# Kernel optimization log

Hardware: AMD Instinct MI355X
Metric: run time of the kernel (lower is better)

Reference implementation:

```python
import jax, jax.numpy as jnp
import numpy as np

EPS = 1e-5

def conv3x3(x, w, b):
    # x: [B,C,H,W], w: [O,I,3,3]
    y = jax.lax.conv_general_dilated(x, w, window_strides=(1, 1),
                                     padding=((1, 1), (1, 1)),
                                     dimension_numbers=('NCHW', 'OIHW', 'NCHW'))
    return y + b[None, :, None, None]

def batchnorm(x, gamma, beta):
    # training-mode BN: batch stats over (N,H,W), biased variance
    mean = jnp.mean(x, axis=(0, 2, 3), keepdims=True)
    var = jnp.mean((x - mean) ** 2, axis=(0, 2, 3), keepdims=True)
    xn = (x - mean) * jax.lax.rsqrt(var + EPS)
    return xn * gamma[None, :, None, None] + beta[None, :, None, None]

def setup_inputs() -> dict:
    key = jax.random.key(0)
    ks = jax.random.split(key, 5)
    B, C, H, W = 4, 256, 64, 64
    fan = C * 9
    return {
        'x': jax.random.normal(ks[0], (B, C, H, W), jnp.float32),
        'wv': jax.random.normal(ks[1], (C, C, 3, 3), jnp.float32) / np.sqrt(fan),
        'bv': jax.random.normal(ks[2], (C,), jnp.float32) * 0.01,
        'gv': jnp.ones((C,), jnp.float32),
        'betav': jnp.zeros((C,), jnp.float32),
        'ww': jax.random.normal(ks[3], (C, C, 3, 3), jnp.float32) / np.sqrt(fan),
        'bw': jax.random.normal(ks[4], (C,), jnp.float32) * 0.01,
        'gw': jnp.ones((C,), jnp.float32),
        'betaw': jnp.zeros((C,), jnp.float32),
    }

def reference(x, wv, bv, gv, betav, ww, bw, gw, betaw):
    B, C, H, W = x.shape
    N = H * W
    # value branch: conv3x3 + BN -> [B, N, C]
    value = batchnorm(conv3x3(x, wv, bv), gv, betav).reshape(B, C, N)
    key_ = x.reshape(B, C, N)              # [B, C, N]
    query = key_.transpose(0, 2, 1)        # [B, N, C]
    sim = jnp.einsum('bnc,bcm->bnm', query, key_) * (C ** -0.5)  # [B, N, N]
    sim = jax.nn.softmax(sim, axis=-1)
    context = jnp.einsum('bnm,bcm->bcn', sim, value)             # [B, C, N]
    context = context.reshape(B, C, H, W)
    out = jax.nn.relu(batchnorm(conv3x3(context, ww, bw), gw, betaw))
    return out
```

## Files before the change

kernel.cpp:

```cpp
#include <hip/hip_runtime.h>
#include <cstdint>
#include <cstddef>

typedef __attribute__((ext_vector_type(8))) __bf16 bf16x8;
typedef __attribute__((ext_vector_type(4))) __bf16 bf16x4;
typedef __attribute__((ext_vector_type(4))) float  f32x4;

#define NPIX 4096
#define CHN  256

__device__ __forceinline__ void async_copy16(void* lds, const void* g) {
  __builtin_amdgcn_global_load_lds(
      (const __attribute__((address_space(1))) unsigned int*)g,
      (__attribute__((address_space(3))) unsigned int*)lds, 16, 0, 0);
}

__global__ __launch_bounds__(256) void k_transpose_cast(
    const float* __restrict__ X, __bf16* __restrict__ xT)
{
  __shared__ float tile[64][65];
  const int bid = blockIdx.x;
  const int b  = bid >> 8;
  const int pt = (bid >> 2) & 63;
  const int ct = bid & 3;
  const int tid = threadIdx.x;
  const int tc = tid & 63, tr = tid >> 6;
  const float* Xb = X + ((size_t)b*CHN + ct*64)*NPIX + pt*64;
#pragma unroll
  for (int i=0;i<16;++i) {
    int row = tr + i*4;
    tile[row][tc] = Xb[(size_t)row*NPIX + tc];
  }
  __syncthreads();
  __bf16* Tb = xT + ((size_t)b*NPIX + pt*64)*CHN + ct*64;
#pragma unroll
  for (int i=0;i<16;++i) {
    int prow = tr + i*4;
    Tb[(size_t)prow*CHN + tc] = (__bf16)tile[tc][prow];
  }
}

__global__ __launch_bounds__(256) void k_wcast(
    const float* __restrict__ wv, const float* __restrict__ ww,
    __bf16* __restrict__ wvt, __bf16* __restrict__ wwt)
{
  int idx = blockIdx.x*256 + threadIdx.x;
  int t = idx >> 16;
  int o = (idx >> 8) & 255;
  int i = idx & 255;
  size_t src = ((size_t)o*256 + i)*9 + t;
  wvt[idx] = (__bf16)wv[src];
  wwt[idx] = (__bf16)ww[src];
}

__global__ __launch_bounds__(512, 1) void k_conv_tap(
    const __bf16* __restrict__ W9,
    const __bf16* __restrict__ Bt,
    const __bf16* __restrict__ zb,
    __bf16* __restrict__ Y)
{
  __shared__ __bf16 Alds[2][128*64];
  __shared__ __bf16 Blds[2][128*64];
  const int bid0 = blockIdx.x;
  const int bid = (bid0 & 7)*32 + (bid0 >> 3);
  const int b  = bid >> 6;
  const int mt = (bid >> 5) & 1;
  const int nt = bid & 31;
  const int m0 = mt << 7;
  const int p0 = nt << 7;
  const int tid = threadIdx.x;
  const int w = tid >> 6, l = tid & 63;
  const int l15 = l & 15, lhi = l >> 4;
  const int wr = (w >> 1) << 5;
  const int wc = (w & 1) << 6;

  const __bf16* Btb = Bt + ((size_t)b << 20);
  const f32x4 vzero = {0.f,0.f,0.f,0.f};
  f32x4 acc[2][4];
#pragma unroll
  for (int i=0;i<2;++i)
#pragma unroll
    for (int j=0;j<4;++j) acc[i][j] = vzero;

  auto stage = [&](int buf, int it) {
    const int t = it >> 2, kc = it & 3;
    const int dy = t/3 - 1, dx = t%3 - 1;
    const int dq = dy*64 + dx;
    const int k0 = kc << 6;
#pragma unroll
    for (int i=0;i<2;++i) {
      int inst = w*2 + i;
      int s = inst*64 + l;
      int row = s >> 3, ch = s & 7;
      const __bf16* g = W9 + (size_t)t*65536 + (size_t)(m0+row)*256 + k0
                        + ((ch ^ (row & 7)) << 3);
      async_copy16((char*)(&Alds[buf][0]) + inst*1024, g);
    }
#pragma unroll
    for (int i=0;i<2;++i) {
      int inst = w*2 + i;
      int s = inst*64 + l;
      int pp = s >> 3, ch = s & 7;
      int p = p0 + pp;
      int xx = (p & 63) + dx;
      int yy = (p >> 6) + dy;
      bool ok = ((unsigned)xx < 64u) & ((unsigned)yy < 64u);
      const __bf16* g = ok ? (Btb + (size_t)(p + dq)*256 + k0 + ((ch ^ (pp & 7)) << 3))
                           : zb;
      async_copy16((char*)(&Blds[buf][0]) + inst*1024, g);
    }
  };

  stage(0, 0);
#pragma unroll 1
  for (int it=0; it<36; ++it) {
    const int cur = it & 1;
    if (it < 35) {
      stage(cur^1, it+1);
      asm volatile("s_waitcnt vmcnt(4)" ::: "memory");
    } else {
      asm volatile("s_waitcnt vmcnt(0)" ::: "memory");
    }
    __builtin_amdgcn_s_barrier();
    __builtin_amdgcn_sched_barrier(0);

    const char* Ac = (const char*)(&Alds[cur][0]);
    const char* Bc = (const char*)(&Blds[cur][0]);
#pragma unroll
    for (int kk=0; kk<2; ++kk) {
      const int swz = (((kk<<2)+lhi) ^ (l15 & 7)) << 4;
      bf16x8 af[2], bfr[4];
#pragma unroll
      for (int i=0;i<2;++i)
        af[i] = *(const bf16x8*)(Ac + (size_t)(wr + 16*i + l15)*128 + swz);
#pragma unroll
      for (int j=0;j<4;++j)
        bfr[j] = *(const bf16x8*)(Bc + (size_t)(wc + 16*j + l15)*128 + swz);
#pragma unroll
      for (int i=0;i<2;++i)
#pragma unroll
        for (int j=0;j<4;++j)
          acc[i][j] = __builtin_amdgcn_mfma_f32_16x16x32_bf16(af[i], bfr[j], acc[i][j], 0,0,0);
    }
    __builtin_amdgcn_s_barrier();
  }

  __bf16* Yb = Y + ((size_t)b << 20);
#pragma unroll
  for (int i=0;i<2;++i)
#pragma unroll
    for (int j=0;j<4;++j)
#pragma unroll
      for (int r=0;r<4;++r) {
        int row = m0 + wr + 16*i + lhi*4 + r;
        int col = p0 + wc + 16*j + l15;
        Yb[(size_t)row*NPIX + col] = (__bf16)acc[i][j][r];
      }
}

__global__ __launch_bounds__(256) void k_bn_stats(
    const __bf16* __restrict__ Y, const float* __restrict__ gamma,
    const float* __restrict__ beta, float* __restrict__ scale,
    float* __restrict__ shift)
{
  const int c = blockIdx.x;
  const int tid = threadIdx.x;
  float s = 0.f, s2 = 0.f;
#pragma unroll 1
  for (int b=0;b<4;++b) {
    const __bf16* p = Y + ((size_t)b*CHN + c)*NPIX;
#pragma unroll
    for (int i=0;i<2;++i) {
      bf16x8 v = *(const bf16x8*)(p + (tid + i*256)*8);
#pragma unroll
      for (int j=0;j<8;++j) { float f = (float)v[j]; s += f; s2 += f*f; }
    }
  }
#pragma unroll
  for (int d=1; d<64; d<<=1) { s += __shfl_xor(s, d, 64); s2 += __shfl_xor(s2, d, 64); }
  __shared__ float rs[4], rs2[4];
  if ((tid & 63) == 0) { rs[tid>>6] = s; rs2[tid>>6] = s2; }
  __syncthreads();
  if (tid == 0) {
    float S  = rs[0]+rs[1]+rs[2]+rs[3];
    float S2 = rs2[0]+rs2[1]+rs2[2]+rs2[3];
    const float inv_n = 1.f/16384.f;
    float mean = S*inv_n;
    float var  = S2*inv_n - mean*mean;
    float rstd = rsqrtf(var + 1e-5f);
    float sc = gamma[c]*rstd;
    scale[c] = sc;
    shift[c] = beta[c] - mean*sc;
  }
}

__global__ __launch_bounds__(256) void k_bn_relu(
    const __bf16* __restrict__ Y, const float* __restrict__ scale,
    const float* __restrict__ shift, float* __restrict__ out)
{
  size_t idx = ((size_t)blockIdx.x*256 + threadIdx.x)*8;
  int c = (int)((idx >> 12) & 255);
  bf16x8 v = *(const bf16x8*)(Y + idx);
  float sc = scale[c], sh = shift[c];
  float4 r0, r1;
  r0.x = fmaxf((float)v[0]*sc + sh, 0.f);
  r0.y = fmaxf((float)v[1]*sc + sh, 0.f);
  r0.z = fmaxf((float)v[2]*sc + sh, 0.f);
  r0.w = fmaxf((float)v[3]*sc + sh, 0.f);
  r1.x = fmaxf((float)v[4]*sc + sh, 0.f);
  r1.y = fmaxf((float)v[5]*sc + sh, 0.f);
  r1.z = fmaxf((float)v[6]*sc + sh, 0.f);
  r1.w = fmaxf((float)v[7]*sc + sh, 0.f);
  *(float4*)(out + idx)     = r0;
  *(float4*)(out + idx + 4) = r1;
}

__global__ __launch_bounds__(512, 2) void k_attn(
    const __bf16* __restrict__ xT,
    const __bf16* __restrict__ val,
    const float* __restrict__ scale,
    const float* __restrict__ shift,
    __bf16* __restrict__ O)
{
  __shared__ __align__(16) char smem[141312];

  const int bid0 = blockIdx.x;
  const int bid = (bid0 & 7)*32 + (bid0 >> 3);
  const int b  = bid >> 6;
  const int q0 = (bid & 63) << 6;
  const int tid = threadIdx.x;
  const int w = tid >> 6, l = tid & 63;
  const int l15 = l & 15, lhi = l >> 4;
  const int qh  = w & 1;
  const int kvq = w >> 1;
  const int p   = kvq >> 1;
  const int cfh = kvq & 1;

  const __bf16* xTb = xT  + ((size_t)b << 20);
  const __bf16* vb  = val + ((size_t)b << 20);

  bf16x8 aq[2][8];
#pragma unroll
  for (int rg=0; rg<2; ++rg) {
    const __bf16* qp = xTb + (size_t)(q0 + qh*32 + rg*16 + l15)*256 + lhi*8;
#pragma unroll
    for (int kc=0; kc<8; ++kc) {
      bf16x8 v = *(const bf16x8*)(qp + kc*32);
#pragma unroll
      for (int j=0;j<8;++j) v[j] = (__bf16)((float)v[j] * 0.0625f);
      aq[rg][kc] = v;
    }
  }

  auto stage = [&](int buf, int m0) {
    char* kb = smem + buf*32768;
    char* vv = smem + 65536 + buf*32768;
#pragma unroll
    for (int i=0;i<4;++i) {
      int inst = w*4 + i;
      int s = inst*64 + l;
      int row = s >> 5, cs = s & 31;
      const __bf16* g = xTb + (size_t)(m0 + row)*256 + ((cs ^ (row & 7)) << 3);
      async_copy16(kb + inst*1024, g);
    }
#pragma unroll
    for (int i=0;i<4;++i) {
      int inst = w*4 + i;
      int s = inst*64 + l;
      int row = s >> 3, cs = s & 7;
      const __bf16* g = vb + (size_t)row*NPIX + m0 + ((cs ^ (row & 7)) << 3);
      async_copy16(vv + inst*1024, g);
    }
  };

  const f32x4 vzero = {0.f,0.f,0.f,0.f};
  float lsum[2][4];
#pragma unroll
  for (int rg=0;rg<2;++rg)
#pragma unroll
    for (int r=0;r<4;++r) lsum[rg][r] = 0.f;
  f32x4 o[2][8];
#pragma unroll
  for (int rg=0;rg<2;++rg)
#pragma unroll
    for (int cf=0; cf<8; ++cf) o[rg][cf] = vzero;

  stage(0, 0);

#pragma unroll 1
  for (int mt=0; mt<64; ++mt) {
    const int cur = mt & 1;
    asm volatile("s_waitcnt vmcnt(0)" ::: "memory");
    __builtin_amdgcn_s_barrier();
    __builtin_amdgcn_sched_barrier(0);
    if (mt < 63) stage(cur^1, (mt+1) << 6);

    const char* Kc = smem + cur*32768;
    const char* Vc = smem + 65536 + cur*32768;
    __bf16* pReg = (__bf16*)(smem + 131072 + (qh*2 + p)*2560);

    f32x4 s4[2];
    s4[0] = vzero; s4[1] = vzero;
    {
      const int krow = kvq*16 + l15;
      const char* kbase = Kc + krow*512;
#pragma unroll
      for (int kc=0; kc<8; ++kc) {
        bf16x8 bk = *(const bf16x8*)(kbase + ((((kc<<2)+lhi) ^ (krow&7)) << 4));
        s4[0] = __builtin_amdgcn_mfma_f32_16x16x32_bf16(aq[0][kc], bk, s4[0], 0,0,0);
        s4[1] = __builtin_amdgcn_mfma_f32_16x16x32_bf16(aq[1][kc], bk, s4[1], 0,0,0);
      }
    }

#pragma unroll
    for (int rg=0;rg<2;++rg)
#pragma unroll
      for (int r=0;r<4;++r) {
        float pv = __expf(s4[rg][r]);
        __bf16 pbf = (__bf16)pv;
        pReg[(rg*16 + lhi*4 + r)*40 + cfh*16 + l15] = pbf;
        lsum[rg][r] += (float)pbf;
      }

    asm volatile("s_waitcnt lgkmcnt(0)" ::: "memory");
    __builtin_amdgcn_s_barrier();
    __builtin_amdgcn_sched_barrier(0);

    bf16x8 pa0 = *(const bf16x8*)(pReg + (size_t)l15*40 + lhi*8);
    bf16x8 pa1 = *(const bf16x8*)(pReg + (size_t)(16 + l15)*40 + lhi*8);

#pragma unroll
    for (int cf=0; cf<8; ++cf) {
      const int c = cfh*128 + (cf<<4) + l15;
      const char* vbase = Vc + c*128;
      bf16x8 bv = *(const bf16x8*)(vbase + ((((p<<2)+lhi) ^ (c&7)) << 4));
      o[0][cf] = __builtin_amdgcn_mfma_f32_16x16x32_bf16(pa0, bv, o[0][cf], 0,0,0);
      o[1][cf] = __builtin_amdgcn_mfma_f32_16x16x32_bf16(pa1, bv, o[1][cf], 0,0,0);
    }
  }

#pragma unroll
  for (int rg=0;rg<2;++rg)
#pragma unroll
    for (int r=0;r<4;++r)
#pragma unroll
      for (int d=1; d<16; d<<=1) lsum[rg][r] += __shfl_xor(lsum[rg][r], d, 64);

  __builtin_amdgcn_s_barrier();
  float* oscr = (float*)smem;
  float* lscr = (float*)(smem + 65536);
  if (l15 == 0) {
#pragma unroll
    for (int rg=0;rg<2;++rg)
#pragma unroll
      for (int r=0;r<4;++r)
        lscr[w*32 + rg*16 + lhi*4 + r] = lsum[rg][r];
  }
  if (p == 1) {
    float* od = oscr + (size_t)(qh*2 + cfh)*4096;
#pragma unroll
    for (int rg=0;rg<2;++rg)
#pragma unroll
      for (int cf=0;cf<8;++cf)
#pragma unroll
        for (int r=0;r<4;++r)
          od[(rg*16 + lhi*4 + r)*128 + (cf<<4) + l15] = o[rg][cf][r];
  }
  asm volatile("s_waitcnt lgkmcnt(0)" ::: "memory");
  __builtin_amdgcn_s_barrier();
  if (p == 0) {
    const float* od = oscr + (size_t)(qh*2 + cfh)*4096;
    __bf16* Ob = O + ((size_t)b << 20);
#pragma unroll
    for (int rg=0;rg<2;++rg) {
      float inv[4];
#pragma unroll
      for (int r=0;r<4;++r) {
        float tot = 0.f;
#pragma unroll
        for (int k=0;k<4;++k)
          tot += lscr[(qh + 2*k)*32 + rg*16 + lhi*4 + r];
        inv[r] = 1.f / tot;
      }
#pragma unroll
      for (int cf=0;cf<8;++cf) {
        const int c = cfh*128 + (cf<<4) + l15;
        const float sc = scale[c], sh = shift[c];
#pragma unroll
        for (int r=0;r<4;++r) {
          float vtot = o[rg][cf][r] + od[(rg*16 + lhi*4 + r)*128 + (cf<<4) + l15];
          int row = q0 + qh*32 + rg*16 + lhi*4 + r;
          Ob[(size_t)row*256 + c] = (__bf16)(vtot * inv[r] * sc + sh);
        }
      }
    }
  }
}

extern "C" void kernel_launch(void* const* d_in, const int* in_sizes, int n_in,
                              void* d_out, int out_size, void* d_ws, size_t ws_size,
                              hipStream_t stream)
{
  const float* x     = (const float*)d_in[0];
  const float* wv    = (const float*)d_in[1];
  const float* gv    = (const float*)d_in[3];
  const float* betav = (const float*)d_in[4];
  const float* ww    = (const float*)d_in[5];
  const float* gw    = (const float*)d_in[7];
  const float* betaw = (const float*)d_in[8];
  float* out = (float*)d_out;

  char* ws = (char*)d_ws;
  __bf16* xT     = (__bf16*)(ws);
  __bf16* Obuf   = (__bf16*)(ws + 8388608);
  __bf16* ybuf   = (__bf16*)(ws + 16777216);
  __bf16* wvt    = (__bf16*)(ws + 25165824);
  __bf16* wwt    = (__bf16*)(ws + 26345472);
  float* scale_v = (float*)(ws + 27525120);
  float* shift_v = (float*)(ws + 27526144);
  float* scale_w = (float*)(ws + 27527168);
  float* shift_w = (float*)(ws + 27528192);
  __bf16* zbuf   = (__bf16*)(ws + 27529216);
  if (ws_size < 27530240) return;

  hipMemsetAsync(zbuf, 0, 1024, stream);

  k_transpose_cast<<<1024, 256, 0, stream>>>(x, xT);
  k_wcast<<<2304, 256, 0, stream>>>(wv, ww, wvt, wwt);

  k_conv_tap<<<256, 512, 0, stream>>>(wvt, xT, zbuf, ybuf);
  k_bn_stats<<<256, 256, 0, stream>>>(ybuf, gv, betav, scale_v, shift_v);

  k_attn<<<256, 512, 0, stream>>>(xT, ybuf, scale_v, shift_v, Obuf);

  k_conv_tap<<<256, 512, 0, stream>>>(wwt, Obuf, zbuf, ybuf);
  k_bn_stats<<<256, 256, 0, stream>>>(ybuf, gw, betaw, scale_w, shift_w);
  k_bn_relu<<<2048, 256, 0, stream>>>(ybuf, scale_w, shift_w, out);
}
```

Baseline: 197.3 us.

## Fuse BN partial statistics into conv epilogue and finalize with tiny kernel

The conv kernel now accumulates per-channel sum and sum-of-squares of its bf16-rounded outputs, reduces them across lanes with shuffles, and writes per-tile partials to workspace. A single-block finalize kernel sums the 256 partials per channel to produce scale and shift. This replaces the separate BN stats kernel that re-read the whole 8MB conv output. It adds shuffle reductions to the conv epilogue and a serial 256-iteration loop in a one-block kernel.

```diff
diff --git a/kernel.cpp b/kernel.cpp
--- a/kernel.cpp
+++ b/kernel.cpp
@@ -57,7 +57,9 @@
     const __bf16* __restrict__ W9,
     const __bf16* __restrict__ Bt,
     const __bf16* __restrict__ zb,
-    __bf16* __restrict__ Y)
+    __bf16* __restrict__ Y,
+    float* __restrict__ PS,
+    float* __restrict__ PS2)
 {
   __shared__ __bf16 Alds[2][128*64];
   __shared__ __bf16 Blds[2][128*64];
@@ -146,6 +148,11 @@
   }
 
   __bf16* Yb = Y + ((size_t)b << 20);
+  float ps[2][4], ps2[2][4];
+#pragma unroll
+  for (int i=0;i<2;++i)
+#pragma unroll
+    for (int r=0;r<4;++r) { ps[i][r] = 0.f; ps2[i][r] = 0.f; }
 #pragma unroll
   for (int i=0;i<2;++i)
 #pragma unroll
@@ -154,44 +161,53 @@
       for (int r=0;r<4;++r) {
         int row = m0 + wr + 16*i + lhi*4 + r;
         int col = p0 + wc + 16*j + l15;
-        Yb[(size_t)row*NPIX + col] = (__bf16)acc[i][j][r];
-      }
-}
-
-__global__ __launch_bounds__(256) void k_bn_stats(
-    const __bf16* __restrict__ Y, const float* __restrict__ gamma,
-    const float* __restrict__ beta, float* __restrict__ scale,
-    float* __restrict__ shift)
-{
-  const int c = blockIdx.x;
-  const int tid = threadIdx.x;
-  float s = 0.f, s2 = 0.f;
-#pragma unroll 1
-  for (int b=0;b<4;++b) {
-    const __bf16* p = Y + ((size_t)b*CHN + c)*NPIX;
-#pragma unroll
-    for (int i=0;i<2;++i) {
-      bf16x8 v = *(const bf16x8*)(p + (tid + i*256)*8);
-#pragma unroll
-      for (int j=0;j<8;++j) { float f = (float)v[j]; s += f; s2 += f*f; }
-    }
-  }
-#pragma unroll
-  for (int d=1; d<64; d<<=1) { s += __shfl_xor(s, d, 64); s2 += __shfl_xor(s2, d, 64); }
-  __shared__ float rs[4], rs2[4];
-  if ((tid & 63) == 0) { rs[tid>>6] = s; rs2[tid>>6] = s2; }
-  __syncthreads();
-  if (tid == 0) {
-    float S  = rs[0]+rs[1]+rs[2]+rs[3];
-    float S2 = rs2[0]+rs2[1]+rs2[2]+rs2[3];
-    const float inv_n = 1.f/16384.f;
-    float mean = S*inv_n;
-    float var  = S2*inv_n - mean*mean;
-    float rstd = rsqrtf(var + 1e-5f);
-    float sc = gamma[c]*rstd;
-    scale[c] = sc;
-    shift[c] = beta[c] - mean*sc;
-  }
+        __bf16 vb16 = (__bf16)acc[i][j][r];
+        float v = (float)vb16;
+        ps[i][r]  += v;
+        ps2[i][r] += v*v;
+        Yb[(size_t)row*NPIX + col] = vb16;
+      }
+#pragma unroll
+  for (int i=0;i<2;++i)
+#pragma unroll
+    for (int r=0;r<4;++r)
+#pragma unroll
+      for (int d=1; d<16; d<<=1) {
+        ps[i][r]  += __shfl_xor(ps[i][r],  d, 64);
+        ps2[i][r] += __shfl_xor(ps2[i][r], d, 64);
+      }
+  if (l15 == 0) {
+    const int contrib = b*64 + nt*2 + (wc >> 6);
+#pragma unroll
+    for (int i=0;i<2;++i)
+#pragma unroll
+      for (int r=0;r<4;++r) {
+        int c = m0 + wr + 16*i + lhi*4 + r;
+        PS [contrib*256 + c] = ps[i][r];
+        PS2[contrib*256 + c] = ps2[i][r];
+      }
+  }
+}
+
+__global__ __launch_bounds__(256) void k_bn_finalize(
+    const float* __restrict__ PS, const float* __restrict__ PS2,
+    const float* __restrict__ gamma, const float* __restrict__ beta,
+    float* __restrict__ scale, float* __restrict__ shift)
+{
+  const int c = threadIdx.x;
+  float S = 0.f, S2 = 0.f;
+#pragma unroll 4
+  for (int k=0;k<256;++k) {
+    S  += PS [k*256 + c];
+    S2 += PS2[k*256 + c];
+  }
+  const float inv_n = 1.f/16384.f;
+  float mean = S*inv_n;
+  float var  = S2*inv_n - mean*mean;
+  float rstd = rsqrtf(var + 1e-5f);
+  float sc = gamma[c]*rstd;
+  scale[c] = sc;
+  shift[c] = beta[c] - mean*sc;
 }
 
 __global__ __launch_bounds__(256) void k_bn_relu(
@@ -421,19 +437,21 @@
   float* scale_w = (float*)(ws + 27527168);
   float* shift_w = (float*)(ws + 27528192);
   __bf16* zbuf   = (__bf16*)(ws + 27529216);
-  if (ws_size < 27530240) return;
+  float* part_s  = (float*)(ws + 27530240);
+  float* part_s2 = (float*)(ws + 27792384);
+  if (ws_size < 28054528) return;
 
   hipMemsetAsync(zbuf, 0, 1024, stream);
 
   k_transpose_cast<<<1024, 256, 0, stream>>>(x, xT);
   k_wcast<<<2304, 256, 0, stream>>>(wv, ww, wvt, wwt);
 
-  k_conv_tap<<<256, 512, 0, stream>>>(wvt, xT, zbuf, ybuf);
-  k_bn_stats<<<256, 256, 0, stream>>>(ybuf, gv, betav, scale_v, shift_v);
+  k_conv_tap<<<256, 512, 0, stream>>>(wvt, xT, zbuf, ybuf, part_s, part_s2);
+  k_bn_finalize<<<1, 256, 0, stream>>>(part_s, part_s2, gv, betav, scale_v, shift_v);
 
   k_attn<<<256, 512, 0, stream>>>(xT, ybuf, scale_v, shift_v, Obuf);
 
-  k_conv_tap<<<256, 512, 0, stream>>>(wwt, Obuf, zbuf, ybuf);
-  k_bn_stats<<<256, 256, 0, stream>>>(ybuf, gw, betaw, scale_w, shift_w);
+  k_conv_tap<<<256, 512, 0, stream>>>(wwt, Obuf, zbuf, ybuf, part_s, part_s2);
+  k_bn_finalize<<<1, 256, 0, stream>>>(part_s, part_s2, gw, betaw, scale_w, shift_w);
   k_bn_relu<<<2048, 256, 0, stream>>>(ybuf, scale_w, shift_w, out);
 }
```

Measured after the change: 237.5 us. 20.4% more time.
